# Kernel tuning notes

Hardware: AMD Instinct MI355X
Metric: run time of the kernel (lower is better)

Reference implementation:

```python
import jax, jax.numpy as jnp
import numpy as np
import math

MASK_FILL = -1e6  # d2l masked_softmax fills masked scores with -1e6


def setup_inputs() -> dict:
    key = jax.random.key(0)
    kq, kk, kv, kl = jax.random.split(key, 4)
    B, Lq, Lk, D = 16, 2048, 2048, 64
    queries = jax.random.normal(kq, (B, Lq, D), dtype=jnp.float32)
    keys = jax.random.normal(kk, (B, Lk, D), dtype=jnp.float32)
    values = jax.random.normal(kv, (B, Lk, D), dtype=jnp.float32)
    valid_lens = jax.random.randint(kl, (B,), 1, Lk + 1, dtype=jnp.int32)
    return {"queries": queries, "keys": keys, "values": values, "valid_lens": valid_lens}


def reference(queries, keys, values, valid_lens):
    # scores: [B, Lq, Lk]
    d = queries.shape[-1]
    scores = jnp.einsum("bqd,bkd->bqk", queries, keys) / math.sqrt(d)
    # masked_softmax: positions >= valid_lens[b] along key axis get -1e6
    Lk = keys.shape[1]
    mask = jnp.arange(Lk)[None, None, :] < valid_lens[:, None, None]  # [B,1,Lk]
    scores = jnp.where(mask, scores, MASK_FILL)
    attn = jax.nn.softmax(scores, axis=-1)
    # dropout p=0.0 (eval) is identity
    return jnp.einsum("bqk,bkd->bqd", attn, values)
```

## Files before the change

### kernel.cpp

```cpp
#include <hip/hip_runtime.h>
#include <hip/hip_bf16.h>
#include <stdint.h>


#define BATCH 16
#define SEQ   2048
#define DIM   64
#define NSPLIT 4
#define NTHR  256

typedef __bf16 bf16x8 __attribute__((ext_vector_type(8)));
typedef float  f32x16 __attribute__((ext_vector_type(16)));
typedef unsigned int u32x2 __attribute__((ext_vector_type(2)));

static constexpr float QSCALE = 0.125f * 1.44269504088896340736f;

__device__ __forceinline__ uint32_t pk2bf(float a, float b) {
    union { __hip_bfloat162 h; uint32_t u; } c;
    c.h = __float22bfloat162_rn(make_float2(a, b));
    return c.u;
}
__device__ __forceinline__ bf16x8 mk8(uint32_t w0, uint32_t w1, uint32_t w2, uint32_t w3) {
    union { uint32_t u[4]; bf16x8 v; } c;
    c.u[0] = w0; c.u[1] = w1; c.u[2] = w2; c.u[3] = w3;
    return c.v;
}
__device__ __forceinline__ u32x2 plswap(uint32_t a, uint32_t b) {
    return __builtin_amdgcn_permlane32_swap(a, b, false, false);
}
__device__ __forceinline__ float vmax16(const f32x16& v) {
    float a = fmaxf(fmaxf(v[0], v[1]), fmaxf(v[2], v[3]));
    float b = fmaxf(fmaxf(v[4], v[5]), fmaxf(v[6], v[7]));
    float c = fmaxf(fmaxf(v[8], v[9]), fmaxf(v[10], v[11]));
    float d = fmaxf(fmaxf(v[12], v[13]), fmaxf(v[14], v[15]));
    return fmaxf(fmaxf(a, b), fmaxf(c, d));
}
__device__ __forceinline__ float vsum16(const f32x16& v) {
    float a = (v[0] + v[1]) + (v[2] + v[3]);
    float b = (v[4] + v[5]) + (v[6] + v[7]);
    float c = (v[8] + v[9]) + (v[10] + v[11]);
    float d = (v[12] + v[13]) + (v[14] + v[15]);
    return (a + b) + (c + d);
}

__global__ __launch_bounds__(256) void prep_kv(
        const float* __restrict__ K, const float* __restrict__ V,
        unsigned short* __restrict__ Kbf, unsigned short* __restrict__ Vt)
{
    __shared__ float tl[64][65];
    const int bid = blockIdx.x;
    const int b  = bid >> 5;
    const int kb = (bid & 31) * 64;
    const int tid = threadIdx.x;

    const float* Kp = K + ((size_t)b * SEQ + kb) * DIM;
    const float* Vp = V + ((size_t)b * SEQ + kb) * DIM;
    unsigned short* Ko = Kbf + ((size_t)b * SEQ + kb) * DIM;
    unsigned short* Vo = Vt + (size_t)b * SEQ * DIM + (size_t)(kb >> 5) * 2048;

    #pragma unroll
    for (int p = 0; p < 4; ++p) {
        int idx = p * 256 + tid;
        float4 x = ((const float4*)Kp)[idx];
        ((uint2*)Ko)[idx] = make_uint2(pk2bf(x.x, x.y), pk2bf(x.z, x.w));
    }
    #pragma unroll
    for (int p = 0; p < 4; ++p) {
        int idx = p * 256 + tid;
        int r = idx >> 4, c = (idx & 15) * 4;
        float4 x = *(const float4*)(Vp + r * DIM + c);
        tl[r][c] = x.x; tl[r][c+1] = x.y; tl[r][c+2] = x.z; tl[r][c+3] = x.w;
    }
    __syncthreads();
    #pragma unroll
    for (int p = 0; p < 4; ++p) {
        int idx = p * 256 + tid;
        int sub = idx >> 9;
        int rem = idx & 511;
        int d  = rem >> 3;
        int kq = (rem & 7) * 4;
        int kr = sub * 32 + kq;
        *(uint2*)(Vo + sub * 2048 + d * 32 + kq) =
            make_uint2(pk2bf(tl[kr][d],     tl[kr + 1][d]),
                       pk2bf(tl[kr + 2][d], tl[kr + 3][d]));
    }
}

__global__ __launch_bounds__(NTHR, 2) void attn_main(
        const float* __restrict__ Q, const unsigned short* __restrict__ Kbf,
        const unsigned short* __restrict__ Vt, const int* __restrict__ VL,
        float* __restrict__ O)
{
    __shared__ float comb[NSPLIT - 1][64 * 64 + 256];

    const int tid  = threadIdx.x;
    const int idx  = blockIdx.x;
    const int b    = ((idx & 15) + (idx >> 8)) & (BATCH - 1);
    const int qt   = (idx >> 4) & 31;
    const int qb   = qt * 64;
    const int split = tid >> 6;
    const int lane = tid & 63;
    const int h    = lane >> 5;
    const int ln   = lane & 31;

    const int valid  = VL[b];
    const int ntiles = (valid + 31) >> 5;

    const size_t bOff = (size_t)b * SEQ * DIM;

    bf16x8 qfA[4], qfB[4];
    {
        const float* qpA = Q + bOff + (size_t)(qb + ln) * DIM;
        const float* qpB = Q + bOff + (size_t)(qb + 32 + ln) * DIM;
        #pragma unroll
        for (int s = 0; s < 4; ++s) {
            int c0 = s * 16 + h * 8;
            float4 xa = *(const float4*)(qpA + c0);
            float4 ya = *(const float4*)(qpA + c0 + 4);
            qfA[s] = mk8(pk2bf(xa.x * QSCALE, xa.y * QSCALE),
                         pk2bf(xa.z * QSCALE, xa.w * QSCALE),
                         pk2bf(ya.x * QSCALE, ya.y * QSCALE),
                         pk2bf(ya.z * QSCALE, ya.w * QSCALE));
            float4 xb = *(const float4*)(qpB + c0);
            float4 yb = *(const float4*)(qpB + c0 + 4);
            qfB[s] = mk8(pk2bf(xb.x * QSCALE, xb.y * QSCALE),
                         pk2bf(xb.z * QSCALE, xb.w * QSCALE),
                         pk2bf(yb.x * QSCALE, yb.y * QSCALE),
                         pk2bf(yb.z * QSCALE, yb.w * QSCALE));
        }
    }

    f32x16 oA0, oA1, oB0, oB1;
    #pragma unroll
    for (int r = 0; r < 16; ++r) { oA0[r] = 0.0f; oA1[r] = 0.0f; oB0[r] = 0.0f; oB1[r] = 0.0f; }
    float mA = -1e30f, lA = 0.0f, mB = -1e30f, lB = 0.0f;

    const unsigned short* kp = Kbf + bOff + (size_t)ln * DIM + h * 8;
    const unsigned short* vp = Vt  + bOff + (size_t)ln * 32  + h * 8;

    bf16x8 ka[4], va[4];
    int kt = split;
    if (kt < ntiles) {
        const unsigned short* kq = kp + (size_t)kt * 2048;
        const unsigned short* vq = vp + (size_t)kt * 2048;
        #pragma unroll
        for (int s = 0; s < 4; ++s) ka[s] = *(const bf16x8*)(kq + s * 16);
        va[0] = *(const bf16x8*)(vq);
        va[1] = *(const bf16x8*)(vq + 16);
        va[2] = *(const bf16x8*)(vq + 1024);
        va[3] = *(const bf16x8*)(vq + 1024 + 16);
    }

    for (; kt < ntiles; kt += NSPLIT) {
        const int ktn = (kt + NSPLIT < ntiles) ? kt + NSPLIT : kt;
        bf16x8 kan[4], van[4];
        {
            const unsigned short* kq = kp + (size_t)ktn * 2048;
            const unsigned short* vq = vp + (size_t)ktn * 2048;
            #pragma unroll
            for (int s = 0; s < 4; ++s) kan[s] = *(const bf16x8*)(kq + s * 16);
            van[0] = *(const bf16x8*)(vq);
            van[1] = *(const bf16x8*)(vq + 16);
            van[2] = *(const bf16x8*)(vq + 1024);
            van[3] = *(const bf16x8*)(vq + 1024 + 16);
        }

        f32x16 stA, stB;
        #pragma unroll
        for (int r = 0; r < 16; ++r) { stA[r] = 0.0f; stB[r] = 0.0f; }
        #pragma unroll
        for (int s = 0; s < 4; ++s) {
            stA = __builtin_amdgcn_mfma_f32_32x32x16_bf16(ka[s], qfA[s], stA, 0, 0, 0);
            stB = __builtin_amdgcn_mfma_f32_32x32x16_bf16(ka[s], qfB[s], stB, 0, 0, 0);
        }

        const int kb = kt * 32;
        if (kb + 32 > valid) {
            #pragma unroll
            for (int r = 0; r < 16; ++r) {
                int krel = (r & 3) + 8 * (r >> 2) + 4 * h;
                if (kb + krel >= valid) { stA[r] = -1e30f; stB[r] = -1e30f; }
            }
        }

        float pmA = vmax16(stA);
        float pmB = vmax16(stB);
        u32x2 smA = plswap(__float_as_uint(pmA), __float_as_uint(pmA));
        u32x2 smB = plswap(__float_as_uint(pmB), __float_as_uint(pmB));
        pmA = fmaxf(__uint_as_float(smA[0]), __uint_as_float(smA[1]));
        pmB = fmaxf(__uint_as_float(smB[0]), __uint_as_float(smB[1]));
        if (!__all(pmA <= mA + 8.0f)) {
            float mn = fmaxf(mA, pmA);
            float sc = __builtin_exp2f(mA - mn);
            lA *= sc;
            #pragma unroll
            for (int r = 0; r < 16; ++r) { oA0[r] *= sc; oA1[r] *= sc; }
            mA = mn;
        }
        if (!__all(pmB <= mB + 8.0f)) {
            float mn = fmaxf(mB, pmB);
            float sc = __builtin_exp2f(mB - mn);
            lB *= sc;
            #pragma unroll
            for (int r = 0; r < 16; ++r) { oB0[r] *= sc; oB1[r] *= sc; }
            mB = mn;
        }
        #pragma unroll
        for (int r = 0; r < 16; ++r) {
            stA[r] = __builtin_exp2f(stA[r] - mA);
            stB[r] = __builtin_exp2f(stB[r] - mB);
        }
        float psA = vsum16(stA);
        float psB = vsum16(stB);
        u32x2 ssA = plswap(__float_as_uint(psA), __float_as_uint(psA));
        u32x2 ssB = plswap(__float_as_uint(psB), __float_as_uint(psB));
        lA += __uint_as_float(ssA[0]) + __uint_as_float(ssA[1]);
        lB += __uint_as_float(ssB[0]) + __uint_as_float(ssB[1]);

        bf16x8 bpA0, bpA1, bpB0, bpB1;
        {
            uint32_t u0 = pk2bf(stA[0],  stA[1]),  u1 = pk2bf(stA[2],  stA[3]);
            uint32_t u2 = pk2bf(stA[4],  stA[5]),  u3 = pk2bf(stA[6],  stA[7]);
            uint32_t u4 = pk2bf(stA[8],  stA[9]),  u5 = pk2bf(stA[10], stA[11]);
            uint32_t u6 = pk2bf(stA[12], stA[13]), u7 = pk2bf(stA[14], stA[15]);
            u32x2 sA = plswap(u0, u2), sB = plswap(u1, u3);
            bpA0 = mk8(sA[0], sB[0], sA[1], sB[1]);
            u32x2 sC = plswap(u4, u6), sD = plswap(u5, u7);
            bpA1 = mk8(sC[0], sD[0], sC[1], sD[1]);
        }
        {
            uint32_t u0 = pk2bf(stB[0],  stB[1]),  u1 = pk2bf(stB[2],  stB[3]);
            uint32_t u2 = pk2bf(stB[4],  stB[5]),  u3 = pk2bf(stB[6],  stB[7]);
            uint32_t u4 = pk2bf(stB[8],  stB[9]),  u5 = pk2bf(stB[10], stB[11]);
            uint32_t u6 = pk2bf(stB[12], stB[13]), u7 = pk2bf(stB[14], stB[15]);
            u32x2 sA = plswap(u0, u2), sB = plswap(u1, u3);
            bpB0 = mk8(sA[0], sB[0], sA[1], sB[1]);
            u32x2 sC = plswap(u4, u6), sD = plswap(u5, u7);
            bpB1 = mk8(sC[0], sD[0], sC[1], sD[1]);
        }

        oA0 = __builtin_amdgcn_mfma_f32_32x32x16_bf16(va[0], bpA0, oA0, 0, 0, 0);
        oB0 = __builtin_amdgcn_mfma_f32_32x32x16_bf16(va[0], bpB0, oB0, 0, 0, 0);
        oA1 = __builtin_amdgcn_mfma_f32_32x32x16_bf16(va[2], bpA0, oA1, 0, 0, 0);
        oB1 = __builtin_amdgcn_mfma_f32_32x32x16_bf16(va[2], bpB0, oB1, 0, 0, 0);
        oA0 = __builtin_amdgcn_mfma_f32_32x32x16_bf16(va[1], bpA1, oA0, 0, 0, 0);
        oB0 = __builtin_amdgcn_mfma_f32_32x32x16_bf16(va[1], bpB1, oB0, 0, 0, 0);
        oA1 = __builtin_amdgcn_mfma_f32_32x32x16_bf16(va[3], bpA1, oA1, 0, 0, 0);
        oB1 = __builtin_amdgcn_mfma_f32_32x32x16_bf16(va[3], bpB1, oB1, 0, 0, 0);

        #pragma unroll
        for (int i = 0; i < 4; ++i) { ka[i] = kan[i]; va[i] = van[i]; }
    }

    if (split != 0) {
        float* base = comb[split - 1];
        #pragma unroll
        for (int r = 0; r < 16; ++r) {
            base[r * 64 + lane]        = oA0[r];
            base[(r + 16) * 64 + lane] = oA1[r];
            base[(r + 32) * 64 + lane] = oB0[r];
            base[(r + 48) * 64 + lane] = oB1[r];
        }
        base[4096 + lane]       = mA;
        base[4096 + 64 + lane]  = lA;
        base[4096 + 128 + lane] = mB;
        base[4096 + 192 + lane] = lB;
    }
    __syncthreads();
    if (split == 0) {
        float MA = mA, MB = mB;
        #pragma unroll
        for (int j = 0; j < NSPLIT - 1; ++j) {
            MA = fmaxf(MA, comb[j][4096 + lane]);
            MB = fmaxf(MB, comb[j][4096 + 128 + lane]);
        }
        float scA = __builtin_exp2f(mA - MA), ltA = lA * scA;
        float scB = __builtin_exp2f(mB - MB), ltB = lB * scB;
        #pragma unroll
        for (int r = 0; r < 16; ++r) {
            oA0[r] *= scA; oA1[r] *= scA;
            oB0[r] *= scB; oB1[r] *= scB;
        }
        #pragma unroll
        for (int j = 0; j < NSPLIT - 1; ++j) {
            float mjA = comb[j][4096 + lane];
            float ljA = comb[j][4096 + 64 + lane];
            float mjB = comb[j][4096 + 128 + lane];
            float ljB = comb[j][4096 + 192 + lane];
            float sjA = __builtin_exp2f(mjA - MA);
            float sjB = __builtin_exp2f(mjB - MB);
            ltA += ljA * sjA;
            ltB += ljB * sjB;
            #pragma unroll
            for (int r = 0; r < 16; ++r) {
                oA0[r] += sjA * comb[j][r * 64 + lane];
                oA1[r] += sjA * comb[j][(r + 16) * 64 + lane];
                oB0[r] += sjB * comb[j][(r + 32) * 64 + lane];
                oB1[r] += sjB * comb[j][(r + 48) * 64 + lane];
            }
        }
        float invA = 1.0f / ltA, invB = 1.0f / ltB;
        float* opA = O + bOff + (size_t)(qb + ln) * DIM;
        float* opB = O + bOff + (size_t)(qb + 32 + ln) * DIM;
        #pragma unroll
        for (int a = 0; a < 4; ++a) {
            float4 w;
            w.x = oA0[4*a+0] * invA; w.y = oA0[4*a+1] * invA;
            w.z = oA0[4*a+2] * invA; w.w = oA0[4*a+3] * invA;
            *(float4*)(opA + 8*a + 4*h) = w;
            w.x = oA1[4*a+0] * invA; w.y = oA1[4*a+1] * invA;
            w.z = oA1[4*a+2] * invA; w.w = oA1[4*a+3] * invA;
            *(float4*)(opA + 32 + 8*a + 4*h) = w;
            w.x = oB0[4*a+0] * invB; w.y = oB0[4*a+1] * invB;
            w.z = oB0[4*a+2] * invB; w.w = oB0[4*a+3] * invB;
            *(float4*)(opB + 8*a + 4*h) = w;
            w.x = oB1[4*a+0] * invB; w.y = oB1[4*a+1] * invB;
            w.z = oB1[4*a+2] * invB; w.w = oB1[4*a+3] * invB;
            *(float4*)(opB + 32 + 8*a + 4*h) = w;
        }
    }
}

__device__ __forceinline__ uint32_t swz(uint32_t row, uint32_t colByte) {
    return row * 128u + (colByte ^ ((row & 7u) << 4));
}
__device__ __forceinline__ bf16x8 lds8(const char* p) {
    union { uint4 q; bf16x8 v; } c;
    c.q = *(const uint4*)p;
    return c.v;
}

__global__ __launch_bounds__(256, 2) void attn_fallback(
        const float* __restrict__ Q, const float* __restrict__ K,
        const float* __restrict__ V, const int* __restrict__ VL,
        float* __restrict__ O)
{
    __shared__ unsigned short lds[2][2][64 * DIM];
    const int tid  = threadIdx.x;
    const int bid  = blockIdx.x;
    const int b    = bid & (BATCH - 1);
    const int qt   = bid >> 4;
    const int qb   = qt * 64;
    const int qhalf = (tid >> 6) & 1;
    const int split = tid >> 7;
    const int lane = tid & 63;
    const int h    = lane >> 5;
    const int ln   = lane & 31;
    const int ptid = tid & 127;

    const int valid  = VL[b];
    const int ntiles = (valid + 63) / 64;
    const int nit    = (ntiles + 1) / 2;

    const size_t bOff = (size_t)b * SEQ * DIM;
    const int qrow = qb + qhalf * 32 + ln;

    bf16x8 qf[4];
    {
        const float* qp = Q + bOff + (size_t)qrow * DIM;
        #pragma unroll
        for (int s = 0; s < 4; ++s) {
            int c0 = s * 16 + h * 8;
            float4 x = *(const float4*)(qp + c0);
            float4 y = *(const float4*)(qp + c0 + 4);
            qf[s] = mk8(pk2bf(x.x * QSCALE, x.y * QSCALE),
                        pk2bf(x.z * QSCALE, x.w * QSCALE),
                        pk2bf(y.x * QSCALE, y.y * QSCALE),
                        pk2bf(y.z * QSCALE, y.w * QSCALE));
        }
    }
    f32x16 o0, o1;
    #pragma unroll
    for (int r = 0; r < 16; ++r) { o0[r] = 0.0f; o1[r] = 0.0f; }
    float m_run = -1e30f, l_run = 0.0f;
    const float* Kb = K + bOff;
    const float* Vb = V + bOff;
    char* kls = (char*)lds[split][0];
    char* vls = (char*)lds[split][1];

    for (int it = 0; it < nit; ++it) {
        const int kt = it * 2 + split;
        const bool act = kt < ntiles;
        const int kb = kt * 64;
        if (act) {
            #pragma unroll
            for (int p = 0; p < 8; ++p) {
                int idx = p * 128 + ptid;
                int r = idx >> 4, c = (idx & 15) * 4;
                float4 kx = *(const float4*)(Kb + (size_t)(kb + r) * DIM + c);
                *(uint2*)(kls + swz(r, c * 2)) =
                    make_uint2(pk2bf(kx.x, kx.y), pk2bf(kx.z, kx.w));
            }
            #pragma unroll
            for (int p = 0; p < 2; ++p) {
                int idx = p * 128 + ptid;
                int cq = idx & 15, rq = idx >> 4;
                const float* vp = Vb + (size_t)(kb + rq * 4) * DIM + cq * 4;
                float4 v0 = *(const float4*)(vp);
                float4 v1 = *(const float4*)(vp + DIM);
                float4 v2 = *(const float4*)(vp + 2 * DIM);
                float4 v3 = *(const float4*)(vp + 3 * DIM);
                float a0[4] = {v0.x, v0.y, v0.z, v0.w};
                float a1[4] = {v1.x, v1.y, v1.z, v1.w};
                float a2[4] = {v2.x, v2.y, v2.z, v2.w};
                float a3[4] = {v3.x, v3.y, v3.z, v3.w};
                #pragma unroll
                for (int i = 0; i < 4; ++i)
                    *(uint2*)(vls + swz(cq * 4 + i, rq * 8)) =
                        make_uint2(pk2bf(a0[i], a1[i]), pk2bf(a2[i], a3[i]));
            }
        }
        __syncthreads();
        if (act) {
            f32x16 st0, st1;
            #pragma unroll
            for (int r = 0; r < 16; ++r) { st0[r] = 0.0f; st1[r] = 0.0f; }
            #pragma unroll
            for (int s = 0; s < 4; ++s) {
                int cb = (s * 16 + h * 8) * 2;
                bf16x8 ka0 = lds8(kls + swz(ln,      cb));
                bf16x8 ka1 = lds8(kls + swz(ln + 32, cb));
                st0 = __builtin_amdgcn_mfma_f32_32x32x16_bf16(ka0, qf[s], st0, 0, 0, 0);
                st1 = __builtin_amdgcn_mfma_f32_32x32x16_bf16(ka1, qf[s], st1, 0, 0, 0);
            }
            if (kb + 64 > valid) {
                #pragma unroll
                for (int r = 0; r < 16; ++r) {
                    int krel = (r & 3) + 8 * (r >> 2) + 4 * h;
                    if (kb + krel      >= valid) st0[r] = -1e30f;
                    if (kb + 32 + krel >= valid) st1[r] = -1e30f;
                }
            }
            float pm = fmaxf(vmax16(st0), vmax16(st1));
            u32x2 sm = plswap(__float_as_uint(pm), __float_as_uint(pm));
            pm = fmaxf(__uint_as_float(sm[0]), __uint_as_float(sm[1]));
            float mnew = fmaxf(m_run, pm);
            float sc = __builtin_exp2f(m_run - mnew);
            #pragma unroll
            for (int r = 0; r < 16; ++r) {
                st0[r] = __builtin_exp2f(st0[r] - mnew);
                st1[r] = __builtin_exp2f(st1[r] - mnew);
            }
            float ps = vsum16(st0) + vsum16(st1);
            u32x2 ss = plswap(__float_as_uint(ps), __float_as_uint(ps));
            ps = __uint_as_float(ss[0]) + __uint_as_float(ss[1]);
            l_run = l_run * sc + ps;
            m_run = mnew;
            #pragma unroll
            for (int r = 0; r < 16; ++r) { o0[r] *= sc; o1[r] *= sc; }
            bf16x8 bp[4];
            {
                uint32_t u0 = pk2bf(st0[0], st0[1]),  u1 = pk2bf(st0[2], st0[3]);
                uint32_t u2 = pk2bf(st0[4], st0[5]),  u3 = pk2bf(st0[6], st0[7]);
                uint32_t u4 = pk2bf(st0[8], st0[9]),  u5 = pk2bf(st0[10], st0[11]);
                uint32_t u6 = pk2bf(st0[12], st0[13]), u7 = pk2bf(st0[14], st0[15]);
                u32x2 s02 = plswap(u0, u2), s13 = plswap(u1, u3);
                bp[0] = mk8(s02[0], s13[0], s02[1], s13[1]);
                u32x2 s46 = plswap(u4, u6), s57 = plswap(u5, u7);
                bp[1] = mk8(s46[0], s57[0], s46[1], s57[1]);
            }
            {
                uint32_t u0 = pk2bf(st1[0], st1[1]),  u1 = pk2bf(st1[2], st1[3]);
                uint32_t u2 = pk2bf(st1[4], st1[5]),  u3 = pk2bf(st1[6], st1[7]);
                uint32_t u4 = pk2bf(st1[8], st1[9]),  u5 = pk2bf(st1[10], st1[11]);
                uint32_t u6 = pk2bf(st1[12], st1[13]), u7 = pk2bf(st1[14], st1[15]);
                u32x2 s02 = plswap(u0, u2), s13 = plswap(u1, u3);
                bp[2] = mk8(s02[0], s13[0], s02[1], s13[1]);
                u32x2 s46 = plswap(u4, u6), s57 = plswap(u5, u7);
                bp[3] = mk8(s46[0], s57[0], s46[1], s57[1]);
            }
            #pragma unroll
            for (int x = 0; x < 4; ++x) {
                int cb = (x * 16 + h * 8) * 2;
                bf16x8 va0 = lds8(vls + swz(ln,      cb));
                bf16x8 va1 = lds8(vls + swz(ln + 32, cb));
                o0 = __builtin_amdgcn_mfma_f32_32x32x16_bf16(va0, bp[x], o0, 0, 0, 0);
                o1 = __builtin_amdgcn_mfma_f32_32x32x16_bf16(va1, bp[x], o1, 0, 0, 0);
            }
        }
        __syncthreads();
    }
    const int CSTRIDE = 32 * 64 + 128;
    float* comb = (float*)lds;
    if (split != 0) {
        float* base = comb + (size_t)qhalf * CSTRIDE;
        #pragma unroll
        for (int r = 0; r < 16; ++r) {
            base[r * 64 + lane]        = o0[r];
            base[(r + 16) * 64 + lane] = o1[r];
        }
        base[2048 + lane]      = m_run;
        base[2048 + 64 + lane] = l_run;
    }
    __syncthreads();
    if (split == 0) {
        float* base = comb + (size_t)qhalf * CSTRIDE;
        float mj = base[2048 + lane];
        float lj = base[2048 + 64 + lane];
        float M  = fmaxf(m_run, mj);
        float sc0 = __builtin_exp2f(m_run - M);
        float scj = __builtin_exp2f(mj - M);
        float lt = l_run * sc0 + lj * scj;
        float inv = 1.0f / lt;
        float* op = O + bOff + (size_t)qrow * DIM;
        #pragma unroll
        for (int a = 0; a < 4; ++a) {
            float4 w0, w1;
            w0.x = (o0[4*a+0]*sc0 + scj*base[(4*a+0)*64 + lane]) * inv;
            w0.y = (o0[4*a+1]*sc0 + scj*base[(4*a+1)*64 + lane]) * inv;
            w0.z = (o0[4*a+2]*sc0 + scj*base[(4*a+2)*64 + lane]) * inv;
            w0.w = (o0[4*a+3]*sc0 + scj*base[(4*a+3)*64 + lane]) * inv;
            w1.x = (o1[4*a+0]*sc0 + scj*base[(4*a+16)*64 + lane]) * inv;
            w1.y = (o1[4*a+1]*sc0 + scj*base[(4*a+17)*64 + lane]) * inv;
            w1.z = (o1[4*a+2]*sc0 + scj*base[(4*a+18)*64 + lane]) * inv;
            w1.w = (o1[4*a+3]*sc0 + scj*base[(4*a+19)*64 + lane]) * inv;
            *(float4*)(op + 8*a + 4*h)      = w0;
            *(float4*)(op + 32 + 8*a + 4*h) = w1;
        }
    }
}

extern "C" void kernel_launch(void* const* d_in, const int* in_sizes, int n_in,
                              void* d_out, int out_size, void* d_ws, size_t ws_size,
                              hipStream_t stream) {
    const float* q  = (const float*)d_in[0];
    const float* k  = (const float*)d_in[1];
    const float* v  = (const float*)d_in[2];
    const int*   vl = (const int*)d_in[3];
    float* out = (float*)d_out;

    const size_t KBYTES = (size_t)BATCH * SEQ * DIM * 2;
    if (ws_size >= 2 * KBYTES) {
        unsigned short* kbf = (unsigned short*)d_ws;
        unsigned short* vt  = (unsigned short*)((char*)d_ws + KBYTES);
        hipLaunchKernelGGL(prep_kv, dim3(BATCH * (SEQ / 64)), dim3(256), 0, stream,
                           k, v, kbf, vt);
        hipLaunchKernelGGL(attn_main, dim3(BATCH * (SEQ / 64)), dim3(NTHR), 0, stream,
                           q, kbf, vt, vl, out);
    } else {
        hipLaunchKernelGGL(attn_fallback, dim3(BATCH * (SEQ / 64)), dim3(256), 0, stream,
                           q, k, v, vl, out);
    }
}
```

Before: 42.37 us.

## Split key range into two halves across blocks and merge partials

The attention kernel now launches twice as many blocks, each covering half of the key tiles (split-K across blocks), and writes unnormalized partial outputs plus running max and sum to workspace. A new merge kernel combines the two halves with log-sum-exp rescaling and writes the final output. This aims to raise occupancy and balance load across 512 blocks on a GPU with many CUs, especially given varying valid lengths. It costs an extra kernel launch and extra global traffic for partial results, and second-half blocks for short sequences do no useful work.

```diff
diff --git a/kernel.cpp b/kernel.cpp
--- a/kernel.cpp
+++ b/kernel.cpp
@@ -89,14 +89,17 @@
 __global__ __launch_bounds__(NTHR, 2) void attn_main(
         const float* __restrict__ Q, const unsigned short* __restrict__ Kbf,
         const unsigned short* __restrict__ Vt, const int* __restrict__ VL,
-        float* __restrict__ O)
+        float* __restrict__ PO, float* __restrict__ PM, float* __restrict__ PL)
 {
     __shared__ float comb[NSPLIT - 1][64 * 64 + 256];
 
     const int tid  = threadIdx.x;
     const int idx  = blockIdx.x;
-    const int b    = ((idx & 15) + (idx >> 8)) & (BATCH - 1);
-    const int qt   = (idx >> 4) & 31;
+    const int g    = idx >> 8;
+    const int u    = idx & 255;
+    const int b    = ((u & 15) + g) & (BATCH - 1);
+    const int qt   = ((g & 1) << 4) + (u >> 4);
+    const int half = g >> 1;
     const int qb   = qt * 64;
     const int split = tid >> 6;
     const int lane = tid & 63;
@@ -105,6 +108,8 @@
 
     const int valid  = VL[b];
     const int ntiles = (valid + 31) >> 5;
+    const int lo = half * 32;
+    const int hi = (ntiles < lo + 32) ? ntiles : lo + 32;
 
     const size_t bOff = (size_t)b * SEQ * DIM;
 
@@ -139,8 +144,8 @@
     const unsigned short* vp = Vt  + bOff + (size_t)ln * 32  + h * 8;
 
     bf16x8 ka[4], va[4];
-    int kt = split;
-    if (kt < ntiles) {
+    int kt = lo + split;
+    if (kt < hi) {
         const unsigned short* kq = kp + (size_t)kt * 2048;
         const unsigned short* vq = vp + (size_t)kt * 2048;
         #pragma unroll
@@ -151,8 +156,8 @@
         va[3] = *(const bf16x8*)(vq + 1024 + 16);
     }
 
-    for (; kt < ntiles; kt += NSPLIT) {
-        const int ktn = (kt + NSPLIT < ntiles) ? kt + NSPLIT : kt;
+    for (; kt < hi; kt += NSPLIT) {
+        const int ktn = (kt + NSPLIT < hi) ? kt + NSPLIT : kt;
         bf16x8 kan[4], van[4];
         {
             const unsigned short* kq = kp + (size_t)ktn * 2048;
@@ -299,25 +304,62 @@
                 oB1[r] += sjB * comb[j][(r + 48) * 64 + lane];
             }
         }
-        float invA = 1.0f / ltA, invB = 1.0f / ltB;
-        float* opA = O + bOff + (size_t)(qb + ln) * DIM;
-        float* opB = O + bOff + (size_t)(qb + 32 + ln) * DIM;
+        const int p = (b * 32 + qt) * 2 + half;
+        float* poP = PO + (size_t)p * 4096;
         #pragma unroll
         for (int a = 0; a < 4; ++a) {
             float4 w;
-            w.x = oA0[4*a+0] * invA; w.y = oA0[4*a+1] * invA;
-            w.z = oA0[4*a+2] * invA; w.w = oA0[4*a+3] * invA;
-            *(float4*)(opA + 8*a + 4*h) = w;
-            w.x = oA1[4*a+0] * invA; w.y = oA1[4*a+1] * invA;
-            w.z = oA1[4*a+2] * invA; w.w = oA1[4*a+3] * invA;
-            *(float4*)(opA + 32 + 8*a + 4*h) = w;
-            w.x = oB0[4*a+0] * invB; w.y = oB0[4*a+1] * invB;
-            w.z = oB0[4*a+2] * invB; w.w = oB0[4*a+3] * invB;
-            *(float4*)(opB + 8*a + 4*h) = w;
-            w.x = oB1[4*a+0] * invB; w.y = oB1[4*a+1] * invB;
-            w.z = oB1[4*a+2] * invB; w.w = oB1[4*a+3] * invB;
-            *(float4*)(opB + 32 + 8*a + 4*h) = w;
-        }
+            w.x = oA0[4*a+0]; w.y = oA0[4*a+1]; w.z = oA0[4*a+2]; w.w = oA0[4*a+3];
+            *(float4*)(poP + ln * 64 + 8*a + 4*h) = w;
+            w.x = oA1[4*a+0]; w.y = oA1[4*a+1]; w.z = oA1[4*a+2]; w.w = oA1[4*a+3];
+            *(float4*)(poP + ln * 64 + 32 + 8*a + 4*h) = w;
+            w.x = oB0[4*a+0]; w.y = oB0[4*a+1]; w.z = oB0[4*a+2]; w.w = oB0[4*a+3];
+            *(float4*)(poP + (32 + ln) * 64 + 8*a + 4*h) = w;
+            w.x = oB1[4*a+0]; w.y = oB1[4*a+1]; w.z = oB1[4*a+2]; w.w = oB1[4*a+3];
+            *(float4*)(poP + (32 + ln) * 64 + 32 + 8*a + 4*h) = w;
+        }
+        if (h == 0) {
+            PM[(size_t)p * 64 + ln]      = MA;
+            PL[(size_t)p * 64 + ln]      = ltA;
+            PM[(size_t)p * 64 + 32 + ln] = MB;
+            PL[(size_t)p * 64 + 32 + ln] = ltB;
+        }
+    }
+}
+
+__global__ __launch_bounds__(256) void merge_halves(
+        const float* __restrict__ PO, const float* __restrict__ PM,
+        const float* __restrict__ PL, float* __restrict__ O)
+{
+    const int mb = blockIdx.x;
+    const int b  = mb & (BATCH - 1);
+    const int qt = mb >> 4;
+    const int p0 = (b * 32 + qt) * 2;
+    const int p1 = p0 + 1;
+    const int t  = threadIdx.x;
+    const int row = t >> 2;
+    const int cb  = (t & 3) * 16;
+
+    float m0 = PM[(size_t)p0 * 64 + row], m1 = PM[(size_t)p1 * 64 + row];
+    float l0 = PL[(size_t)p0 * 64 + row], l1 = PL[(size_t)p1 * 64 + row];
+    float M  = fmaxf(m0, m1);
+    float s0 = __builtin_exp2f(m0 - M);
+    float s1 = __builtin_exp2f(m1 - M);
+    float inv = 1.0f / (s0 * l0 + s1 * l1);
+
+    const float* r0 = PO + (size_t)p0 * 4096 + row * 64 + cb;
+    const float* r1 = PO + (size_t)p1 * 4096 + row * 64 + cb;
+    float* out = O + ((size_t)b * SEQ + qt * 64 + row) * DIM + cb;
+    #pragma unroll
+    for (int i = 0; i < 4; ++i) {
+        float4 a = ((const float4*)r0)[i];
+        float4 c = ((const float4*)r1)[i];
+        float4 w;
+        w.x = (s0 * a.x + s1 * c.x) * inv;
+        w.y = (s0 * a.y + s1 * c.y) * inv;
+        w.z = (s0 * a.z + s1 * c.z) * inv;
+        w.w = (s0 * a.w + s1 * c.w) * inv;
+        ((float4*)out)[i] = w;
     }
 }
 
@@ -529,14 +571,21 @@
     const int*   vl = (const int*)d_in[3];
     float* out = (float*)d_out;
 
-    const size_t KBYTES = (size_t)BATCH * SEQ * DIM * 2;
-    if (ws_size >= 2 * KBYTES) {
+    const size_t KBYTES  = (size_t)BATCH * SEQ * DIM * 2;
+    const size_t POBYTES = (size_t)1024 * 4096 * 4;
+    const size_t PMBYTES = (size_t)1024 * 64 * 4;
+    if (ws_size >= 2 * KBYTES + POBYTES + 2 * PMBYTES) {
         unsigned short* kbf = (unsigned short*)d_ws;
         unsigned short* vt  = (unsigned short*)((char*)d_ws + KBYTES);
+        float* po = (float*)((char*)d_ws + 2 * KBYTES);
+        float* pm = (float*)((char*)d_ws + 2 * KBYTES + POBYTES);
+        float* pl = (float*)((char*)d_ws + 2 * KBYTES + POBYTES + PMBYTES);
         hipLaunchKernelGGL(prep_kv, dim3(BATCH * (SEQ / 64)), dim3(256), 0, stream,
                            k, v, kbf, vt);
-        hipLaunchKernelGGL(attn_main, dim3(BATCH * (SEQ / 64)), dim3(NTHR), 0, stream,
-                           q, kbf, vt, vl, out);
+        hipLaunchKernelGGL(attn_main, dim3(1024), dim3(NTHR), 0, stream,
+                           q, kbf, vt, vl, po, pm, pl);
+        hipLaunchKernelGGL(merge_halves, dim3(512), dim3(256), 0, stream,
+                           po, pm, pl, out);
     } else {
         hipLaunchKernelGGL(attn_fallback, dim3(BATCH * (SEQ / 64)), dim3(256), 0, stream,
                            q, k, v, vl, out);
```

New measurement: 51.49 us. 1.22x slower.
